# Kernel optimization log

Hardware: AMD Instinct MI355X
Metric: run time of the kernel (lower is better)

## Reference

```python
import jax, jax.numpy as jnp
import numpy as np

B, N, D = 16, 1024, 1152
H = 16; DH = D // H
GH = GW = 32; SY = SX = 2
WS = SY * SX                      # tokens per window
NW = (GH // SY) * (GW // SX)      # 256 windows (one dst each)
NS = NW * (WS - 1)                # 768 src tokens
NUM_PRUNE = int(N * 0.5)          # 512
NOISE_ALPHA = 0.1
SIM_BETA = 1.0


def setup_inputs() -> dict:
    key = jax.random.key(0)
    ks = jax.random.split(key, 8)
    rn = lambda k, s: jax.random.normal(k, s, jnp.float32) * 0.02
    return dict(
        x=jax.random.normal(ks[0], (B, N, D), jnp.float32),
        noise=jax.random.uniform(ks[1], (B, NW, WS), jnp.float32),
        ln1_g=jnp.ones((D,), jnp.float32), ln1_b=jnp.zeros((D,), jnp.float32),
        ln2_g=jnp.ones((D,), jnp.float32), ln2_b=jnp.zeros((D,), jnp.float32),
        w_qkv=rn(ks[2], (D, 3 * D)), b_qkv=jnp.zeros((3 * D,), jnp.float32),
        w_proj=rn(ks[3], (D, D)), b_proj=jnp.zeros((D,), jnp.float32),
        w_fc1=rn(ks[4], (D, 4 * D)), b_fc1=jnp.zeros((4 * D,), jnp.float32),
        w_fc2=rn(ks[5], (4 * D, D)), b_fc2=jnp.zeros((D,), jnp.float32),
    )


def _ln(x, g, b):
    mu = x.mean(-1, keepdims=True)
    var = ((x - mu) ** 2).mean(-1, keepdims=True)
    return (x - mu) * jax.lax.rsqrt(var + 1e-6) * g + b


def _dit_block(x, ln1_g, ln1_b, ln2_g, ln2_b, w_qkv, b_qkv, w_proj, b_proj,
               w_fc1, b_fc1, w_fc2, b_fc2):
    Bq, T, _ = x.shape
    y = _ln(x, ln1_g, ln1_b)
    q, k, v = jnp.split(y @ w_qkv + b_qkv, 3, axis=-1)
    hd = lambda t: t.reshape(Bq, T, H, DH).transpose(0, 2, 1, 3)  # [B,H,T,DH]
    q, k, v = hd(q), hd(k), hd(v)
    att = jax.nn.softmax(jnp.einsum('bhqd,bhkd->bhqk', q, k) * (1.0 / np.sqrt(DH)), axis=-1)
    o = jnp.einsum('bhqk,bhkd->bhqd', att, v).transpose(0, 2, 1, 3).reshape(Bq, T, D)
    x = x + o @ w_proj + b_proj
    y = _ln(x, ln2_g, ln2_b)
    return x + jax.nn.gelu(y @ w_fc1 + b_fc1) @ w_fc2 + b_fc2


def _sito_indices(x, noise):
    # SiTo seed (dst) selection + similarity-based prune index computation.
    xn = x / (jnp.linalg.norm(x, axis=-1, keepdims=True) + 1e-6)  # cosine feats
    grid = jnp.arange(N).reshape(GH, GW)
    win = grid.reshape(GH // SY, SY, GW // SX, SX).transpose(0, 2, 1, 3).reshape(NW, WS)
    xw = xn[:, win]                                   # [B,NW,WS,D]
    mean = xw.mean(2, keepdims=True)
    score = SIM_BETA * (xw * mean).sum(-1) + NOISE_ALPHA * noise  # [B,NW,WS]
    dst_local = jnp.argmax(score, axis=-1)            # [B,NW]
    winb = jnp.broadcast_to(win, (B, NW, WS))
    dst_idx = jnp.take_along_axis(winb, dst_local[..., None], -1)[..., 0]  # [B,NW]
    local = jnp.arange(WS)[None, None]
    keymat = jnp.where(local != dst_local[..., None], local, WS)
    src_local = jnp.sort(keymat, -1)[..., : WS - 1]   # non-dst locals, in order
    src_idx = jnp.take_along_axis(winb, src_local, -1).reshape(B, NS)
    a = jnp.take_along_axis(xn, src_idx[..., None], 1)      # [B,NS,D]
    bf = jnp.take_along_axis(xn, dst_idx[..., None], 1)     # [B,NW,D]
    sim = jnp.einsum('bsd,bnd->bsn', a, bf)                 # [B,NS,NW]
    best = jnp.argmax(sim, -1)                              # most-similar dst
    order = jnp.argsort(-jnp.max(sim, -1), axis=-1)
    pruned_pos = order[:, :NUM_PRUNE]
    kept_pos = order[:, NUM_PRUNE:]
    src_kept = jnp.take_along_axis(src_idx, kept_pos, 1)
    src_pruned = jnp.take_along_axis(src_idx, pruned_pos, 1)
    pruned_best = jnp.take_along_axis(best, pruned_pos, 1)
    return dst_idx, src_kept, src_pruned, pruned_best


def reference(x, noise, ln1_g, ln1_b, ln2_g, ln2_b, w_qkv, b_qkv, w_proj, b_proj,
              w_fc1, b_fc1, w_fc2, b_fc2):
    dst_idx, src_kept, src_pruned, pruned_best = _sito_indices(x, noise)
    keep_idx = jnp.concatenate([dst_idx, src_kept], axis=1)          # [B,Nk]
    xk = jnp.take_along_axis(x, keep_idx[..., None], 1)              # prune_fn
    out = _dit_block(xk, ln1_g, ln1_b, ln2_g, ln2_b, w_qkv, b_qkv,
                     w_proj, b_proj, w_fc1, b_fc1, w_fc2, b_fc2)

    def recover_one(o, di, sk, sp, pb):  # recover_fn: scatter + copy-from-dst
        out_dst, out_src = o[:NW], o[NW:]
        full = jnp.zeros((N, D), o.dtype)
        full = full.at[di].set(out_dst)
        full = full.at[sk].set(out_src)
        return full.at[sp].set(out_dst[pb])

    return jax.vmap(recover_one)(out, dst_idx, src_kept, src_pruned, pruned_best)
```

## Files before the change

### kernel.cpp

```cpp
#include <hip/hip_runtime.h>
#include <hip/hip_bf16.h>

namespace {

constexpr int Dd = 1152;

typedef __attribute__((ext_vector_type(8))) short bf16x8;
typedef __attribute__((ext_vector_type(4))) float f32x4;

__device__ __forceinline__ void gload_lds16(const void* g, void* l) {
  __builtin_amdgcn_global_load_lds(
      (const __attribute__((address_space(1))) void*)g,
      (__attribute__((address_space(3))) void*)l, 16, 0, 0);
}

__device__ __forceinline__ float gelu_f(float x) {
  float x3 = x * x * x;
  float z2 = 1.5957691216057308f * (x + 0.044715f * x3);
  float e = __expf(fminf(z2, 30.0f));
  return x * e / (e + 1.0f);
}

__global__ __launch_bounds__(256) void normwin_kernel(const float* __restrict__ x,
    const float* __restrict__ noise, float* __restrict__ inv,
    __hip_bfloat16* __restrict__ xnh, __hip_bfloat16* __restrict__ xnl,
    int* __restrict__ dsti, int* __restrict__ srci) {
  const int gidx = blockIdx.x;
  const int b = gidx >> 8, w = gidx & 255;
  const int wy = w >> 4, wx = w & 15;
  const int t0 = wy * 64 + wx * 2;
  const int wid = threadIdx.x >> 6, lane = threadIdx.x & 63;
  const int tok = t0 + (wid >> 1) * 32 + (wid & 1);
  const int row = (b << 10) + tok;

  const float2* xr = (const float2*)(x + (size_t)row * Dd);
  float2 v[9];
  float s = 0.f;
  #pragma unroll
  for (int e = 0; e < 9; ++e) {
    v[e] = xr[lane + 64 * e];
    s += v[e].x * v[e].x + v[e].y * v[e].y;
  }
  #pragma unroll
  for (int m = 1; m < 64; m <<= 1) s += __shfl_xor(s, m);
  float iv = 1.0f / (sqrtf(s) + 1e-6f);
  if (lane == 0) inv[row] = iv;

  __shared__ float2 xns[4][576];
  ushort2* ph = (ushort2*)(xnh + (size_t)row * Dd);
  ushort2* pl = (ushort2*)(xnl + (size_t)row * Dd);
  #pragma unroll
  for (int e = 0; e < 9; ++e) {
    float ax = v[e].x * iv, ay = v[e].y * iv;
    xns[wid][lane + 64 * e] = make_float2(ax, ay);
    __hip_bfloat16 hx = __float2bfloat16(ax), hy = __float2bfloat16(ay);
    __hip_bfloat16 lx = __float2bfloat16(ax - __bfloat162float(hx));
    __hip_bfloat16 ly = __float2bfloat16(ay - __bfloat162float(hy));
    ph[lane + 64 * e] = make_ushort2(*(ushort*)&hx, *(ushort*)&hy);
    pl[lane + 64 * e] = make_ushort2(*(ushort*)&lx, *(ushort*)&ly);
  }
  __syncthreads();

  float dot = 0.f;
  #pragma unroll
  for (int e = 0; e < 9; ++e) {
    int i = lane + 64 * e;
    float2 a0 = xns[0][i], a1 = xns[1][i], a2 = xns[2][i], a3 = xns[3][i];
    float sx = a0.x + a1.x + a2.x + a3.x;
    float sy = a0.y + a1.y + a2.y + a3.y;
    dot += (v[e].x * iv) * sx + (v[e].y * iv) * sy;
  }
  #pragma unroll
  for (int m = 1; m < 64; m <<= 1) dot += __shfl_xor(dot, m);
  __shared__ float dots[4];
  if (lane == 0) dots[wid] = dot;
  __syncthreads();
  if (threadIdx.x == 0) {
    float best = -1e30f; int bj = 0;
    #pragma unroll
    for (int j = 0; j < 4; ++j) {
      float sc = 0.25f * dots[j] + 0.1f * noise[(size_t)gidx * 4 + j];
      if (sc > best) { best = sc; bj = j; }
    }
    int tk[4] = {t0, t0 + 1, t0 + 32, t0 + 33};
    dsti[b * 256 + w] = tk[bj];
    int m = 0;
    #pragma unroll
    for (int j = 0; j < 4; ++j) if (j != bj) srci[b * 768 + w * 3 + (m++)] = tk[j];
  }
}

__global__ __launch_bounds__(256) void simgemm_kernel(
    const __hip_bfloat16* __restrict__ xnh, const __hip_bfloat16* __restrict__ xnl,
    const int* __restrict__ dsti, const int* __restrict__ srci,
    float* __restrict__ mx, int* __restrict__ best) {
  int b = blockIdx.x / 12;
  int m0 = (blockIdx.x % 12) * 64;
  __shared__ __align__(16) __hip_bfloat16 AsH[2][64 * 32];
  __shared__ __align__(16) __hip_bfloat16 AsL[2][64 * 32];
  __shared__ __align__(16) __hip_bfloat16 BsH[2][256 * 32];
  __shared__ __align__(16) __hip_bfloat16 BsL[2][256 * 32];
  const int tid = threadIdx.x, wid = tid >> 6, lane = tid & 63;
  const int g = lane >> 4, lr = lane & 15;

  const int slotRow = tid >> 2;
  const int colByte = (((tid & 3) ^ ((tid >> 3) & 3)) << 4);
  size_t aRow = (size_t)((b << 10) + srci[b * 768 + m0 + slotRow]) * Dd;
  size_t bRow[4];
  #pragma unroll
  for (int p = 0; p < 4; ++p)
    bRow[p] = (size_t)((b << 10) + dsti[b * 256 + p * 64 + slotRow]) * Dd;
  const char* xh = (const char*)xnh;
  const char* xl = (const char*)xnl;

  auto stage = [&](int buf, int k0) {
    size_t ka = (aRow + k0) * 2 + colByte;
    gload_lds16(xh + ka, (char*)AsH + buf * 4096 + wid * 1024);
    gload_lds16(xl + ka, (char*)AsL + buf * 4096 + wid * 1024);
    #pragma unroll
    for (int p = 0; p < 4; ++p) {
      size_t kb = (bRow[p] + k0) * 2 + colByte;
      gload_lds16(xh + kb, (char*)BsH + buf * 16384 + p * 4096 + wid * 1024);
      gload_lds16(xl + kb, (char*)BsL + buf * 16384 + p * 4096 + wid * 1024);
    }
  };

  f32x4 hh[16], hx[16];
  const f32x4 zf = {0.f, 0.f, 0.f, 0.f};
  #pragma unroll
  for (int nf = 0; nf < 16; ++nf) { hh[nf] = zf; hx[nf] = zf; }

  const int roff = ((g ^ ((lr >> 1) & 3)) << 3);
  stage(0, 0);
  asm volatile("s_waitcnt vmcnt(0)" ::: "memory");
  __syncthreads();
  int buf = 0;
  for (int ks = 0; ks < 36; ++ks) {
    if (ks + 1 < 36) stage(buf ^ 1, (ks + 1) * 32);
    bf16x8 ah = *(const bf16x8*)&AsH[buf][(wid * 16 + lr) * 32 + roff];
    bf16x8 al = *(const bf16x8*)&AsL[buf][(wid * 16 + lr) * 32 + roff];
    #pragma unroll
    for (int nf = 0; nf < 16; ++nf) {
      bf16x8 bh = *(const bf16x8*)&BsH[buf][(nf * 16 + lr) * 32 + roff];
      bf16x8 bl = *(const bf16x8*)&BsL[buf][(nf * 16 + lr) * 32 + roff];
      hh[nf] = __builtin_amdgcn_mfma_f32_16x16x32_bf16(ah, bh, hh[nf], 0, 0, 0);
      hx[nf] = __builtin_amdgcn_mfma_f32_16x16x32_bf16(ah, bl, hx[nf], 0, 0, 0);
      hx[nf] = __builtin_amdgcn_mfma_f32_16x16x32_bf16(al, bh, hx[nf], 0, 0, 0);
    }
    asm volatile("s_waitcnt vmcnt(0)" ::: "memory");
    __syncthreads();
    buf ^= 1;
  }

  #pragma unroll
  for (int j = 0; j < 4; ++j) {
    float bv = -1e30f; int bi = 0;
    #pragma unroll
    for (int nf = 0; nf < 16; ++nf) {
      float v = hh[nf][j] + hx[nf][j];
      if (v > bv) { bv = v; bi = nf * 16 + lr; }
    }
    #pragma unroll
    for (int m = 1; m < 16; m <<= 1) {
      float ov = __shfl_xor(bv, m);
      int oi = __shfl_xor(bi, m);
      if (ov > bv || (ov == bv && oi < bi)) { bv = ov; bi = oi; }
    }
    if (lr == 0) {
      int row = m0 + wid * 16 + g * 4 + j;
      mx[b * 768 + row] = bv;
      best[b * 768 + row] = bi;
    }
  }
}

__global__ __launch_bounds__(256) void rank_kernel(const float* __restrict__ mx,
    const int* __restrict__ best, const int* __restrict__ dsti,
    const int* __restrict__ srci, int* __restrict__ keep, int* __restrict__ srow) {
  int b = blockIdx.x;
  int tid = threadIdx.x;
  __shared__ float smx[768];
  for (int i = tid; i < 768; i += 256) smx[i] = mx[b * 768 + i];
  __syncthreads();
  if (tid < 256) {
    int t = dsti[b * 256 + tid];
    keep[b * 512 + tid] = t;
    srow[b * 1024 + t] = tid;
  }
  for (int i = tid; i < 768; i += 256) {
    float v = smx[i];
    int r = 0;
    for (int s = 0; s < 768; ++s) {
      float u = smx[s];
      r += (u > v) || (u == v && s < i);
    }
    int tok = srci[b * 768 + i];
    if (r >= 512) {
      keep[b * 512 + (r - 256)] = tok;
      srow[b * 1024 + tok] = r - 256;
    } else {
      srow[b * 1024 + tok] = best[b * 768 + i];
    }
  }
}

template<int GATHER>
__global__ __launch_bounds__(256) void ln_kernel(const float* __restrict__ xin,
    const int* __restrict__ keep, const float* __restrict__ gw,
    const float* __restrict__ bw, __hip_bfloat16* __restrict__ yout) {
  int row = blockIdx.x;
  const float* xr;
  if (GATHER) {
    int b = row >> 9, t = row & 511;
    int tok = keep[(b << 9) + t];
    xr = xin + (size_t)((b << 10) + tok) * Dd;
  } else {
    xr = xin + (size_t)row * Dd;
  }
  int tid = threadIdx.x;
  float v[5];
  float s = 0.f, s2 = 0.f;
  #pragma unroll
  for (int e = 0; e < 5; ++e) {
    int i = tid + e * 256;
    float val = (i < Dd) ? xr[i] : 0.f;
    v[e] = val; s += val; s2 += val * val;
  }
  #pragma unroll
  for (int m = 1; m < 64; m <<= 1) { s += __shfl_xor(s, m); s2 += __shfl_xor(s2, m); }
  __shared__ float ps[4], ps2[4];
  int wid = tid >> 6, lane = tid & 63;
  if (lane == 0) { ps[wid] = s; ps2[wid] = s2; }
  __syncthreads();
  s = ps[0] + ps[1] + ps[2] + ps[3];
  s2 = ps2[0] + ps2[1] + ps2[2] + ps2[3];
  constexpr float inv_d = 1.0f / Dd;
  float mu = s * inv_d;
  float var = s2 * inv_d - mu * mu;
  float rstd = rsqrtf(var + 1e-6f);
  __hip_bfloat16* yr = yout + (size_t)row * Dd;
  #pragma unroll
  for (int e = 0; e < 5; ++e) {
    int i = tid + e * 256;
    if (i < Dd) {
      yr[i] = __float2bfloat16((v[e] - mu) * rstd * gw[i] + bw[i]);
    }
  }
}

__global__ __launch_bounds__(256) void wtrans_all_kernel(
    const float* __restrict__ w0, __hip_bfloat16* __restrict__ o0,
    const float* __restrict__ w1, __hip_bfloat16* __restrict__ o1,
    const float* __restrict__ w2, __hip_bfloat16* __restrict__ o2,
    const float* __restrict__ w3, __hip_bfloat16* __restrict__ o3) {
  __shared__ float tile[32][33];
  int bid = blockIdx.x;
  const float* w; __hip_bfloat16* wT; int K, N, local;
  if (bid < 3888)       { w = w0; wT = o0; K = 1152; N = 3456; local = bid; }
  else if (bid < 5184)  { w = w1; wT = o1; K = 1152; N = 1152; local = bid - 3888; }
  else if (bid < 10368) { w = w2; wT = o2; K = 1152; N = 4608; local = bid - 5184; }
  else                  { w = w3; wT = o3; K = 4608; N = 1152; local = bid - 10368; }
  int nt = N >> 5;
  int tk = local / nt, tn = local % nt;
  int tid = threadIdx.x;
  #pragma unroll
  for (int e = 0; e < 4; ++e) {
    int idx = tid + e * 256;
    int r = idx >> 5, c = idx & 31;
    tile[r][c] = w[(size_t)(tk * 32 + r) * N + tn * 32 + c];
  }
  __syncthreads();
  #pragma unroll
  for (int e = 0; e < 4; ++e) {
    int idx = tid + e * 256;
    int r = idx >> 5, c = idx & 31;
    wT[(size_t)(tn * 32 + r) * K + tk * 32 + c] = __float2bfloat16(tile[c][r]);
  }
}

template<int EPI>
__device__ __forceinline__ void epi_store(void* C, const float* res, int Nd,
                                          size_t row, size_t col, float v) {
  if (EPI == 0) {
    ((__hip_bfloat16*)C)[row * (size_t)Nd + col] = __float2bfloat16(v);
  } else if (EPI == 1) {
    ((float*)C)[row * (size_t)Nd + col] = v + res[row * (size_t)Nd + col];
  } else if (EPI == 2) {
    ((__hip_bfloat16*)C)[row * (size_t)Nd + col] = __float2bfloat16(gelu_f(v));
  }
}

template<int EPI>
__global__ __launch_bounds__(512, 4) void gemm128_kernel(
    const __hip_bfloat16* __restrict__ A, const __hip_bfloat16* __restrict__ BT,
    const float* __restrict__ bias, const float* __restrict__ res,
    __hip_bfloat16* __restrict__ vTout,
    void* __restrict__ C, int Md, int Nd, int NdPad, int Kd) {
  constexpr int BM = 128;
  __shared__ __align__(16) __hip_bfloat16 As[3][BM * 32];
  __shared__ __align__(16) __hip_bfloat16 Bs[3][256 * 32];
  const int nb = NdPad >> 8;
  const int q8 = gridDim.x >> 3;
  const int wg = (blockIdx.x & 7) * q8 + (blockIdx.x >> 3);
  const int bm = wg / nb, bnb = wg % nb;
  const int tid = threadIdx.x, wid = tid >> 6, lane = tid & 63;
  const int g = lane >> 4, lr = lane & 15;
  const int wm = wid >> 2, wn = wid & 3;
  const size_t m0 = (size_t)bm * BM, n0 = (size_t)bnb * 256;

  const int trow = tid >> 2;
  const int scol = (((tid & 3) ^ ((tid >> 3) & 3)) << 3);
  const char* Ab = (const char*)A;
  const char* Bb = (const char*)BT;

  auto stage = [&](int slot, int kt) {
    const size_t kb = ((size_t)kt << 5) + scol;
    gload_lds16(Ab + (((m0 + trow) * (size_t)Kd + kb) << 1),
                (char*)As + slot * 8192 + wid * 1024);
    gload_lds16(Bb + (((n0 + trow) * (size_t)Kd + kb) << 1),
                (char*)Bs + slot * 16384 + wid * 1024);
    gload_lds16(Bb + (((n0 + 128 + trow) * (size_t)Kd + kb) << 1),
                (char*)Bs + slot * 16384 + 8192 + wid * 1024);
  };

  f32x4 acc[4][4];
  const f32x4 zf = {0.f, 0.f, 0.f, 0.f};
  #pragma unroll
  for (int mi = 0; mi < 4; ++mi)
    #pragma unroll
    for (int ni = 0; ni < 4; ++ni) acc[mi][ni] = zf;

  const int nk = Kd >> 5;
  stage(0, 0);
  stage(1, 1);
  asm volatile("s_waitcnt vmcnt(3)" ::: "memory");
  __builtin_amdgcn_s_barrier();

  int cur = 0;
  const int roff = ((g ^ ((lr >> 1) & 3)) << 3);
  for (int kt = 0; kt < nk; ++kt) {
    const __hip_bfloat16* Ac = As[cur];
    const __hip_bfloat16* Bc = Bs[cur];
    bf16x8 af[4], bf[4];
    #pragma unroll
    for (int mi = 0; mi < 4; ++mi)
      af[mi] = *(const bf16x8*)&Ac[(wm * 64 + mi * 16 + lr) * 32 + roff];
    #pragma unroll
    for (int ni = 0; ni < 4; ++ni)
      bf[ni] = *(const bf16x8*)&Bc[(wn * 64 + ni * 16 + lr) * 32 + roff];
    if (kt + 2 < nk) stage(cur == 0 ? 2 : cur - 1, kt + 2);
    __builtin_amdgcn_s_barrier();
    __builtin_amdgcn_s_setprio(1);
    #pragma unroll
    for (int mi = 0; mi < 4; ++mi)
      #pragma unroll
      for (int ni = 0; ni < 4; ++ni)
        acc[mi][ni] = __builtin_amdgcn_mfma_f32_16x16x32_bf16(af[mi], bf[ni], acc[mi][ni], 0, 0, 0);
    __builtin_amdgcn_s_setprio(0);
    if (kt + 2 < nk)      asm volatile("s_waitcnt vmcnt(3)" ::: "memory");
    else if (kt + 1 < nk) asm volatile("s_waitcnt vmcnt(0)" ::: "memory");
    __builtin_amdgcn_s_barrier();
    cur = (cur == 2) ? 0 : cur + 1;
  }

  #pragma unroll
  for (int ni = 0; ni < 4; ++ni) {
    size_t col = n0 + wn * 64 + ni * 16 + lr;
    if (col < (size_t)Nd) {
      float bv = bias[col];
      if (EPI == 4 && col >= 2304) {
        int vc = (int)col - 2304;
        int h = vc / 72, d = vc % 72;
        #pragma unroll
        for (int mi = 0; mi < 4; ++mi) {
          #pragma unroll
          for (int j = 0; j < 4; ++j) {
            size_t row = m0 + wm * 64 + mi * 16 + g * 4 + j;
            int bb = (int)(row >> 9), t = (int)(row & 511);
            vTout[(((size_t)(bb * 16 + h)) * 80 + d) * 512 + t] =
                __float2bfloat16(acc[mi][ni][j] + bv);
          }
        }
      } else {
        #pragma unroll
        for (int mi = 0; mi < 4; ++mi) {
          #pragma unroll
          for (int j = 0; j < 4; ++j) {
            size_t row = m0 + wm * 64 + mi * 16 + g * 4 + j;
            float v = acc[mi][ni][j] + bv;
            if (EPI == 4) {
              ((__hip_bfloat16*)C)[row * (size_t)Nd + col] = __float2bfloat16(v);
            } else {
              epi_store<EPI>(C, res, Nd, row, col, v);
            }
          }
        }
      }
    }
  }
}

template<int EPI>
__global__ __launch_bounds__(256, 3) void gemm128v_kernel(
    const __hip_bfloat16* __restrict__ A, const __hip_bfloat16* __restrict__ BT,
    const float* __restrict__ bias, const float* __restrict__ res,
    const int* __restrict__ keepIdx, const float* __restrict__ xsrc,
    void* __restrict__ C, int Md, int Nd, int Kd) {
  __shared__ __align__(16) __hip_bfloat16 As[3][128 * 32];
  __shared__ __align__(16) __hip_bfloat16 Bs[3][128 * 32];
  const int nb = Nd >> 7;
  const int q8 = gridDim.x >> 3;
  const int wg = (blockIdx.x & 7) * q8 + (blockIdx.x >> 3);
  const int bm = wg / nb, bnb = wg % nb;
  const int tid = threadIdx.x, wid = tid >> 6, lane = tid & 63;
  const int g = lane >> 4, lr = lane & 15;
  const int wm = wid >> 1, wn = wid & 1;
  const size_t m0 = (size_t)bm * 128, n0 = (size_t)bnb * 128;

  const int trow = tid >> 2;
  const int scol = (((tid & 3) ^ ((tid >> 3) & 3)) << 3);
  const char* Ab = (const char*)A;
  const char* Bb = (const char*)BT;

  auto stage = [&](int slot, int kt) {
    const size_t kb = ((size_t)kt << 5) + scol;
    #pragma unroll
    for (int c = 0; c < 2; ++c)
      gload_lds16(Ab + (((m0 + c * 64 + trow) * (size_t)Kd + kb) << 1),
                  (char*)As + slot * 8192 + c * 4096 + tid * 16);
    #pragma unroll
    for (int c = 0; c < 2; ++c)
      gload_lds16(Bb + (((n0 + c * 64 + trow) * (size_t)Kd + kb) << 1),
                  (char*)Bs + slot * 8192 + c * 4096 + tid * 16);
  };

  f32x4 acc[4][4];
  const f32x4 zf = {0.f, 0.f, 0.f, 0.f};
  #pragma unroll
  for (int mi = 0; mi < 4; ++mi)
    #pragma unroll
    for (int ni = 0; ni < 4; ++ni) acc[mi][ni] = zf;

  const int roff = ((g ^ ((lr >> 1) & 3)) << 3);
  const int nk = Kd >> 5;

  bf16x8 afA[4], bfA[4], afB[4], bfB[4];

#define DSREAD(AF, BF, SLOT) { \
  const __hip_bfloat16* Ac_ = As[SLOT]; \
  const __hip_bfloat16* Bc_ = Bs[SLOT]; \
  _Pragma("unroll") for (int mi_ = 0; mi_ < 4; ++mi_) \
    AF[mi_] = *(const bf16x8*)&Ac_[(wm * 64 + mi_ * 16 + lr) * 32 + roff]; \
  _Pragma("unroll") for (int ni_ = 0; ni_ < 4; ++ni_) \
    BF[ni_] = *(const bf16x8*)&Bc_[(wn * 64 + ni_ * 16 + lr) * 32 + roff]; }

#define MFMA16(AF, BF) { \
  __builtin_amdgcn_s_setprio(1); \
  _Pragma("unroll") for (int mi_ = 0; mi_ < 4; ++mi_) \
    _Pragma("unroll") for (int ni_ = 0; ni_ < 4; ++ni_) \
      acc[mi_][ni_] = __builtin_amdgcn_mfma_f32_16x16x32_bf16(AF[mi_], BF[ni_], acc[mi_][ni_], 0, 0, 0); \
  __builtin_amdgcn_s_setprio(0); }

#define GITER(KT, S0, S1, AFC, BFC, AFN, BFN) { \
  if ((KT) <= nk - 3)      { asm volatile("s_waitcnt vmcnt(4)" ::: "memory"); } \
  else if ((KT) == nk - 2) { asm volatile("s_waitcnt vmcnt(0)" ::: "memory"); } \
  asm volatile("s_waitcnt lgkmcnt(0)" ::: "memory"); \
  __builtin_amdgcn_s_barrier(); \
  asm volatile("" ::: "memory"); \
  if ((KT) + 1 < nk) DSREAD(AFN, BFN, (S1)); \
  if ((KT) + 3 < nk) stage((S0), (KT) + 3); \
  MFMA16(AFC, BFC); }

  stage(0, 0); stage(1, 1); stage(2, 2);
  asm volatile("s_waitcnt vmcnt(8)" ::: "memory");
  __builtin_amdgcn_s_barrier();
  asm volatile("" ::: "memory");
  DSREAD(afA, bfA, 0);

  int s0 = 0, s1 = 1;
  for (int kt = 0; kt < nk; kt += 2) {
    GITER(kt, s0, s1, afA, bfA, afB, bfB);
    int s2 = (s1 == 2) ? 0 : s1 + 1;
    GITER(kt + 1, s1, s2, afB, bfB, afA, bfA);
    s0 = s2; s1 = (s2 == 2) ? 0 : s2 + 1;
  }
#undef GITER
#undef MFMA16
#undef DSREAD

  #pragma unroll
  for (int ni = 0; ni < 4; ++ni) {
    size_t col = n0 + wn * 64 + ni * 16 + lr;
    float bv = bias[col];
    #pragma unroll
    for (int mi = 0; mi < 4; ++mi) {
      #pragma unroll
      for (int j = 0; j < 4; ++j) {
        size_t row = m0 + wm * 64 + mi * 16 + g * 4 + j;
        float v = acc[mi][ni][j] + bv;
        if (EPI == 3) {
          int b = (int)(row >> 9);
          int tok = keepIdx[row];
          const float* rr = xsrc + ((size_t)(b << 10) + tok) * Dd;
          ((float*)C)[row * (size_t)Nd + col] = v + rr[col];
        } else {
          epi_store<EPI>(C, res, Nd, row, col, v);
        }
      }
    }
  }
}

__global__ __launch_bounds__(256) void attn_kernel(const __hip_bfloat16* __restrict__ qkv,
    const __hip_bfloat16* __restrict__ vT, __hip_bfloat16* __restrict__ o) {
  const int blk = blockIdx.x;
  const int qp = blk & 3, bh = blk >> 2;
  const int b = bh >> 4, h = bh & 15;
  __shared__ __align__(16) __hip_bfloat16 Qs[128][104];
  __shared__ __align__(16) __hip_bfloat16 Ks[64][104];
  __shared__ __align__(16) __hip_bfloat16 Vs[80][72];
  __shared__ __align__(16) __hip_bfloat16 Ps[4][16][72];
  const int tid = threadIdx.x, wid = tid >> 6, lane = tid & 63;
  const int g = lane >> 4, lr = lane & 15;
  const __hip_bfloat16 zb = __float2bfloat16(0.0f);

  for (int idx = tid; idx < 128 * 18; idx += 256) {
    int r = idx / 18, c = idx % 18;
    *(ushort4*)&Qs[r][c * 4] =
        *(const ushort4*)&qkv[((size_t)(b * 512 + qp * 128 + r)) * 3456 + h * 72 + c * 4];
  }
  for (int idx = tid; idx < 128 * 32; idx += 256) {
    int r = idx / 32, d = 72 + idx % 32;
    Qs[r][d] = zb;
    if (r < 64) Ks[r][d] = zb;
  }
  for (int idx = tid; idx < 8 * 72; idx += 256) {
    Vs[72 + idx / 72][idx % 72] = zb;
  }

  f32x4 ov0[5], ov1[5];
  const f32x4 zf = {0.f, 0.f, 0.f, 0.f};
  #pragma unroll
  for (int ni = 0; ni < 5; ++ni) { ov0[ni] = zf; ov1[ni] = zf; }
  float m0_[4], l0_[4], m1_[4], l1_[4];
  #pragma unroll
  for (int j = 0; j < 4; ++j) {
    m0_[j] = -3.0e38f; l0_[j] = 0.f;
    m1_[j] = -3.0e38f; l1_[j] = 0.f;
  }
  const float scale = 0.11785113019775793f;

  for (int c = 0; c < 8; ++c) {
    __syncthreads();
    for (int idx = tid; idx < 64 * 18; idx += 256) {
      int r = idx / 18, cc = idx % 18;
      *(ushort4*)&Ks[r][cc * 4] =
          *(const ushort4*)&qkv[((size_t)(b * 512 + c * 64 + r)) * 3456 + 1152 + h * 72 + cc * 4];
    }
    for (int idx = tid; idx < 72 * 8; idx += 256) {
      int d = idx >> 3, t8 = idx & 7;
      *(uint4*)&Vs[d][t8 * 8] =
          *(const uint4*)&vT[((size_t)bh * 80 + d) * 512 + c * 64 + t8 * 8];
    }
    __syncthreads();

    #pragma unroll
    for (int qh = 0; qh < 2; ++qh) {
      float* m_ = qh ? m1_ : m0_;
      float* l_ = qh ? l1_ : l0_;
      f32x4* ov = qh ? ov1 : ov0;

      f32x4 sf[4];
      #pragma unroll
      for (int nf = 0; nf < 4; ++nf) sf[nf] = zf;
      #pragma unroll
      for (int ks = 0; ks < 3; ++ks) {
        bf16x8 qa = *(const bf16x8*)&Qs[qh * 64 + wid * 16 + lr][ks * 32 + g * 8];
        #pragma unroll
        for (int nf = 0; nf < 4; ++nf) {
          bf16x8 kb = *(const bf16x8*)&Ks[nf * 16 + lr][ks * 32 + g * 8];
          sf[nf] = __builtin_amdgcn_mfma_f32_16x16x32_bf16(qa, kb, sf[nf], 0, 0, 0);
        }
      }

      float cm[4];
      #pragma unroll
      for (int j = 0; j < 4; ++j)
        cm[j] = fmaxf(fmaxf(sf[0][j], sf[1][j]), fmaxf(sf[2][j], sf[3][j])) * scale;
      #pragma unroll
      for (int mm = 1; mm < 16; mm <<= 1)
        #pragma unroll
        for (int j = 0; j < 4; ++j) cm[j] = fmaxf(cm[j], __shfl_xor(cm[j], mm));
      float fac[4], rs[4];
      #pragma unroll
      for (int j = 0; j < 4; ++j) {
        float nm = fmaxf(m_[j], cm[j]);
        fac[j] = __expf(m_[j] - nm);
        m_[j] = nm;
        rs[j] = 0.f;
      }
      #pragma unroll
      for (int nf = 0; nf < 4; ++nf)
        #pragma unroll
        for (int j = 0; j < 4; ++j) {
          float pv = __expf(sf[nf][j] * scale - m_[j]);
          rs[j] += pv;
          Ps[wid][g * 4 + j][nf * 16 + lr] = __float2bfloat16(pv);
        }
      #pragma unroll
      for (int mm = 1; mm < 16; mm <<= 1)
        #pragma unroll
        for (int j = 0; j < 4; ++j) rs[j] += __shfl_xor(rs[j], mm);
      #pragma unroll
      for (int j = 0; j < 4; ++j) l_[j] = l_[j] * fac[j] + rs[j];
      #pragma unroll
      for (int ni = 0; ni < 5; ++ni)
        #pragma unroll
        for (int j = 0; j < 4; ++j) ov[ni][j] *= fac[j];

      #pragma unroll
      for (int k2 = 0; k2 < 2; ++k2) {
        bf16x8 pa = *(const bf16x8*)&Ps[wid][lr][k2 * 32 + g * 8];
        #pragma unroll
        for (int ni = 0; ni < 5; ++ni) {
          bf16x8 vb = *(const bf16x8*)&Vs[ni * 16 + lr][k2 * 32 + g * 8];
          ov[ni] = __builtin_amdgcn_mfma_f32_16x16x32_bf16(pa, vb, ov[ni], 0, 0, 0);
        }
      }
    }
  }

  #pragma unroll
  for (int qh = 0; qh < 2; ++qh) {
    const f32x4* ov = qh ? ov1 : ov0;
    const float* l_ = qh ? l1_ : l0_;
    #pragma unroll
    for (int ni = 0; ni < 5; ++ni) {
      int d = ni * 16 + lr;
      if (d < 72) {
        #pragma unroll
        for (int j = 0; j < 4; ++j) {
          int t = qp * 128 + qh * 64 + wid * 16 + g * 4 + j;
          o[((size_t)(b * 512 + t)) * 1152 + h * 72 + d] = __float2bfloat16(ov[ni][j] / l_[j]);
        }
      }
    }
  }
}

__global__ __launch_bounds__(256) void recover_kernel(const float* __restrict__ yout,
    const int* __restrict__ srow, float* __restrict__ out) {
  int idx = blockIdx.x * 256 + threadIdx.x;
  int q = idx % 288;
  int bnv = idx / 288;
  int r = srow[bnv];
  int b = bnv >> 10;
  const float4* src = (const float4*)yout + ((size_t)((b << 9) + r)) * 288 + q;
  ((float4*)out)[idx] = *src;
}

}

extern "C" void kernel_launch(void* const* d_in, const int* in_sizes, int n_in,
                              void* d_out, int out_size, void* d_ws, size_t ws_size,
                              hipStream_t stream) {
  (void)in_sizes; (void)n_in; (void)out_size; (void)ws_size;
  const float* x      = (const float*)d_in[0];
  const float* noise  = (const float*)d_in[1];
  const float* ln1_g  = (const float*)d_in[2];
  const float* ln1_b  = (const float*)d_in[3];
  const float* ln2_g  = (const float*)d_in[4];
  const float* ln2_b  = (const float*)d_in[5];
  const float* w_qkv  = (const float*)d_in[6];
  const float* b_qkv  = (const float*)d_in[7];
  const float* w_proj = (const float*)d_in[8];
  const float* b_proj = (const float*)d_in[9];
  const float* w_fc1  = (const float*)d_in[10];
  const float* b_fc1  = (const float*)d_in[11];
  const float* w_fc2  = (const float*)d_in[12];
  const float* b_fc2  = (const float*)d_in[13];
  float* out = (float*)d_out;

  char* p = (char*)d_ws;
  auto alloc = [&](size_t bytes) {
    char* r = p;
    p += (bytes + 255) & ~(size_t)255;
    return r;
  };
  __hip_bfloat16* wqkvT  = (__hip_bfloat16*)alloc((size_t)3584 * 1152 * 2);
  __hip_bfloat16* wprojT = (__hip_bfloat16*)alloc((size_t)1280 * 1152 * 2);
  __hip_bfloat16* wfc1T  = (__hip_bfloat16*)alloc((size_t)4608 * 1152 * 2);
  __hip_bfloat16* wfc2T  = (__hip_bfloat16*)alloc((size_t)1280 * 4608 * 2);
  float* inv = (float*)alloc(16384 * 4);
  int* dsti  = (int*)alloc(4096 * 4);
  int* srci  = (int*)alloc(12288 * 4);
  float* mx  = (float*)alloc(12288 * 4);
  int* best  = (int*)alloc(12288 * 4);
  int* keep  = (int*)alloc(8192 * 4);
  int* srow  = (int*)alloc(16384 * 4);
  float* yout = (float*)alloc((size_t)8192 * 1152 * 4);
  __hip_bfloat16* y1   = (__hip_bfloat16*)alloc((size_t)8192 * 1152 * 2);
  __hip_bfloat16* qkvb = (__hip_bfloat16*)alloc((size_t)8192 * 4608 * 2);
  __hip_bfloat16* vT   = (__hip_bfloat16*)alloc((size_t)256 * 80 * 512 * 2);
  __hip_bfloat16* ob   = (__hip_bfloat16*)alloc((size_t)8192 * 1152 * 2);
  float* x2 = (float*)alloc((size_t)8192 * 1152 * 4);

  __hip_bfloat16* xnh = qkvb;
  __hip_bfloat16* xnl = qkvb + (size_t)16 * 1024 * 1152;

  wtrans_all_kernel<<<15552, 256, 0, stream>>>(w_qkv, wqkvT, w_proj, wprojT,
                                               w_fc1, wfc1T, w_fc2, wfc2T);

  normwin_kernel<<<4096, 256, 0, stream>>>(x, noise, inv, xnh, xnl, dsti, srci);
  simgemm_kernel<<<16 * 12, 256, 0, stream>>>(xnh, xnl, dsti, srci, mx, best);
  rank_kernel<<<16, 256, 0, stream>>>(mx, best, dsti, srci, keep, srow);

  ln_kernel<1><<<8192, 256, 0, stream>>>(x, keep, ln1_g, ln1_b, y1);
  gemm128_kernel<4><<<64 * 14, 512, 0, stream>>>(y1, wqkvT, b_qkv, nullptr, vT,
                                                 qkvb, 8192, 3456, 3584, 1152);
  attn_kernel<<<1024, 256, 0, stream>>>(qkvb, vT, ob);
  gemm128v_kernel<3><<<64 * 9, 256, 0, stream>>>(ob, wprojT, b_proj, nullptr, keep, x,
                                                 x2, 8192, 1152, 1152);
  ln_kernel<0><<<8192, 256, 0, stream>>>(x2, nullptr, ln2_g, ln2_b, y1);
  gemm128v_kernel<2><<<64 * 36, 256, 0, stream>>>(y1, wfc1T, b_fc1, nullptr, nullptr, nullptr,
                                                  qkvb, 8192, 4608, 1152);
  gemm128v_kernel<1><<<64 * 9, 256, 0, stream>>>(qkvb, wfc2T, b_fc2, x2, nullptr, nullptr,
                                                 yout, 8192, 1152, 4608);

  recover_kernel<<<18432, 256, 0, stream>>>(yout, srow, out);
}
```

Before: 697.5 us.

## Triple-buffer similarity GEMM loads with partial vmcnt waits and XCD-aware block remap

Turns the similarity GEMM's double-buffered LDS staging into a three-slot ring with prefetch distance two. Partial vmcnt waits keep the next stage's global-to-LDS loads in flight while the current tile is computed, and s_setprio raises priority around the MFMA loop. Block indices are also remapped so consecutive work groups spread across the 8 XCDs. The cost is more LDS per block, which may lower occupancy, and the hand-counted vmcnt values and the barrier-only synchronisation (no __syncthreads memory fence) are fragile.

Result: no change. 684.0 us (-1.9%).

```diff
diff --git a/kernel.cpp b/kernel.cpp
--- a/kernel.cpp
+++ b/kernel.cpp
@@ -94,12 +94,14 @@
     const __hip_bfloat16* __restrict__ xnh, const __hip_bfloat16* __restrict__ xnl,
     const int* __restrict__ dsti, const int* __restrict__ srci,
     float* __restrict__ mx, int* __restrict__ best) {
-  int b = blockIdx.x / 12;
-  int m0 = (blockIdx.x % 12) * 64;
-  __shared__ __align__(16) __hip_bfloat16 AsH[2][64 * 32];
-  __shared__ __align__(16) __hip_bfloat16 AsL[2][64 * 32];
-  __shared__ __align__(16) __hip_bfloat16 BsH[2][256 * 32];
-  __shared__ __align__(16) __hip_bfloat16 BsL[2][256 * 32];
+  const int q8 = gridDim.x >> 3;
+  const int wg = (blockIdx.x & 7) * q8 + (blockIdx.x >> 3);
+  int b = wg / 12;
+  int m0 = (wg % 12) * 64;
+  __shared__ __align__(16) __hip_bfloat16 AsH[3][64 * 32];
+  __shared__ __align__(16) __hip_bfloat16 AsL[3][64 * 32];
+  __shared__ __align__(16) __hip_bfloat16 BsH[3][256 * 32];
+  __shared__ __align__(16) __hip_bfloat16 BsL[3][256 * 32];
   const int tid = threadIdx.x, wid = tid >> 6, lane = tid & 63;
   const int g = lane >> 4, lr = lane & 15;
 
@@ -113,15 +115,15 @@
   const char* xh = (const char*)xnh;
   const char* xl = (const char*)xnl;
 
-  auto stage = [&](int buf, int k0) {
-    size_t ka = (aRow + k0) * 2 + colByte;
-    gload_lds16(xh + ka, (char*)AsH + buf * 4096 + wid * 1024);
-    gload_lds16(xl + ka, (char*)AsL + buf * 4096 + wid * 1024);
+  auto stage = [&](int slot, int ks) {
+    size_t ka = (aRow + ks * 32) * 2 + colByte;
+    gload_lds16(xh + ka, (char*)AsH + slot * 4096 + wid * 1024);
+    gload_lds16(xl + ka, (char*)AsL + slot * 4096 + wid * 1024);
     #pragma unroll
     for (int p = 0; p < 4; ++p) {
-      size_t kb = (bRow[p] + k0) * 2 + colByte;
-      gload_lds16(xh + kb, (char*)BsH + buf * 16384 + p * 4096 + wid * 1024);
-      gload_lds16(xl + kb, (char*)BsL + buf * 16384 + p * 4096 + wid * 1024);
+      size_t kb = (bRow[p] + ks * 32) * 2 + colByte;
+      gload_lds16(xh + kb, (char*)BsH + slot * 16384 + p * 4096 + wid * 1024);
+      gload_lds16(xl + kb, (char*)BsL + slot * 16384 + p * 4096 + wid * 1024);
     }
   };
 
@@ -132,24 +134,30 @@
 
   const int roff = ((g ^ ((lr >> 1) & 3)) << 3);
   stage(0, 0);
-  asm volatile("s_waitcnt vmcnt(0)" ::: "memory");
-  __syncthreads();
-  int buf = 0;
+  stage(1, 1);
+  asm volatile("s_waitcnt vmcnt(10)" ::: "memory");
+  __builtin_amdgcn_s_barrier();
+
+  int cur = 0;
   for (int ks = 0; ks < 36; ++ks) {
-    if (ks + 1 < 36) stage(buf ^ 1, (ks + 1) * 32);
-    bf16x8 ah = *(const bf16x8*)&AsH[buf][(wid * 16 + lr) * 32 + roff];
-    bf16x8 al = *(const bf16x8*)&AsL[buf][(wid * 16 + lr) * 32 + roff];
+    bf16x8 ah = *(const bf16x8*)&AsH[cur][(wid * 16 + lr) * 32 + roff];
+    bf16x8 al = *(const bf16x8*)&AsL[cur][(wid * 16 + lr) * 32 + roff];
+    if (ks + 2 < 36) stage(cur == 0 ? 2 : cur - 1, ks + 2);
+    __builtin_amdgcn_s_barrier();
+    __builtin_amdgcn_s_setprio(1);
     #pragma unroll
     for (int nf = 0; nf < 16; ++nf) {
-      bf16x8 bh = *(const bf16x8*)&BsH[buf][(nf * 16 + lr) * 32 + roff];
-      bf16x8 bl = *(const bf16x8*)&BsL[buf][(nf * 16 + lr) * 32 + roff];
+      bf16x8 bh = *(const bf16x8*)&BsH[cur][(nf * 16 + lr) * 32 + roff];
+      bf16x8 bl = *(const bf16x8*)&BsL[cur][(nf * 16 + lr) * 32 + roff];
       hh[nf] = __builtin_amdgcn_mfma_f32_16x16x32_bf16(ah, bh, hh[nf], 0, 0, 0);
       hx[nf] = __builtin_amdgcn_mfma_f32_16x16x32_bf16(ah, bl, hx[nf], 0, 0, 0);
       hx[nf] = __builtin_amdgcn_mfma_f32_16x16x32_bf16(al, bh, hx[nf], 0, 0, 0);
     }
-    asm volatile("s_waitcnt vmcnt(0)" ::: "memory");
-    __syncthreads();
-    buf ^= 1;
+    __builtin_amdgcn_s_setprio(0);
+    if (ks + 2 < 36)      asm volatile("s_waitcnt vmcnt(10)" ::: "memory");
+    else if (ks + 1 < 36) asm volatile("s_waitcnt vmcnt(0)" ::: "memory");
+    __builtin_amdgcn_s_barrier();
+    cur = (cur == 2) ? 0 : cur + 1;
   }
 
   #pragma unroll
```
